# Kernel tuning notes

Hardware: AMD Instinct MI355X
Metric: run time of the kernel (lower is better)

The kernel has to match this reference:

```python
import jax, jax.numpy as jnp
import numpy as np

B, L, V, A = 4096, 64, 50000, 1000
E, H, G, F2 = 32, 32, 256, 512


def _xavier(k, shape):
    fan_out, fan_in = shape
    a = np.sqrt(6.0 / (fan_in + fan_out)).astype(np.float32)
    return jax.random.uniform(k, shape, jnp.float32, -a, a)


def setup_inputs() -> dict:
    key = jax.random.key(0)
    ks = jax.random.split(key, 32)
    inp = {}
    inp["q"] = jax.random.randint(ks[0], (B, L), 0, V)
    for i in range(8):
        inp[f"sf{i}"] = jax.random.randint(ks[1 + i], (B, L), 0, V)
    inp["emb"] = _xavier(ks[9], (V, E))
    # torch LSTM weight layout: [4H, in] with gate order i,f,g,o; biases init to 0
    inp["q_Wih"] = _xavier(ks[10], (4 * H, E))
    inp["q_Whh"] = _xavier(ks[11], (4 * H, H))
    inp["q_b"] = jnp.zeros((4 * H,), jnp.float32)
    inp["sf_Wih"] = _xavier(ks[12], (4 * H, E))
    inp["sf_Whh"] = _xavier(ks[13], (4 * H, H))
    inp["sf_b"] = jnp.zeros((4 * H,), jnp.float32)
    inp["g1_W"] = _xavier(ks[14], (G, 2 * H + 1)); inp["g1_b"] = jnp.zeros((G,), jnp.float32)
    inp["g2_W"] = _xavier(ks[15], (G, G)); inp["g2_b"] = jnp.zeros((G,), jnp.float32)
    inp["g3_W"] = _xavier(ks[16], (G, G)); inp["g3_b"] = jnp.zeros((G,), jnp.float32)
    inp["g4_W"] = _xavier(ks[17], (G, G)); inp["g4_b"] = jnp.zeros((G,), jnp.float32)
    inp["f1_W"] = _xavier(ks[18], (G, G)); inp["f1_b"] = jnp.zeros((G,), jnp.float32)
    inp["f2_W"] = _xavier(ks[19], (F2, G)); inp["f2_b"] = jnp.zeros((F2,), jnp.float32)
    inp["f3_W"] = _xavier(ks[20], (A, F2)); inp["f3_b"] = jnp.zeros((A,), jnp.float32)
    return inp


def _lstm_last(x, Wih, Whh, b):
    """x: [L, N, E] -> final hidden state [N, H]. Torch gate order i,f,g,o."""
    n = x.shape[1]
    h_dim = Whh.shape[1]
    def step(carry, xt):
        h, c = carry
        gates = xt @ Wih.T + h @ Whh.T + b  # [N, 4H]
        i, f, g, o = jnp.split(gates, 4, axis=-1)
        c = jax.nn.sigmoid(f) * c + jax.nn.sigmoid(i) * jnp.tanh(g)
        h = jax.nn.sigmoid(o) * jnp.tanh(c)
        return (h, c), None
    init = (jnp.zeros((n, h_dim), x.dtype), jnp.zeros((n, h_dim), x.dtype))
    (h, _), _ = jax.lax.scan(step, init, x)
    return h


def _lin(x, W, b):
    return x @ W.T + b


def reference(q, sf0, sf1, sf2, sf3, sf4, sf5, sf6, sf7,
              emb, q_Wih, q_Whh, q_b, sf_Wih, sf_Whh, sf_b,
              g1_W, g1_b, g2_W, g2_b, g3_W, g3_b, g4_W, g4_b,
              f1_W, f1_b, f2_W, f2_b, f3_W, f3_b):
    # dropout in eval mode (identity)
    b, l = q.shape
    qe = emb[q].transpose(1, 0, 2)  # [L, B, E]
    hq = _lstm_last(qe, q_Wih, q_Whh, q_b)  # [B, H]

    sf = jnp.stack([sf0, sf1, sf2, sf3, sf4, sf5, sf6, sf7])  # [8, B, L]
    sfe = emb[sf]  # [8, B, L, E]
    sfe = sfe.transpose(2, 0, 1, 3).reshape(l, 8 * b, emb.shape[1])  # one fused LSTM over 8*B
    hs = _lstm_last(sfe, sf_Wih, sf_Whh, sf_b).reshape(8, b, -1)  # [8, B, H]

    pos = jnp.broadcast_to(jnp.arange(8, dtype=hs.dtype)[:, None, None], (8, b, 1))
    x = jnp.concatenate([hs, jnp.broadcast_to(hq, (8, b, hq.shape[-1])), pos], axis=-1)  # [8, B, 65]
    x = jax.nn.relu(_lin(x, g1_W, g1_b))
    x = jax.nn.relu(_lin(x, g2_W, g2_b))
    x = jax.nn.relu(_lin(x, g3_W, g3_b))
    x = jax.nn.relu(_lin(x, g4_W, g4_b))
    g_o = x.sum(axis=0)  # [B, 256] segment-sum over the 8 relations

    x = jax.nn.relu(_lin(g_o, f1_W, f1_b))
    x = jax.nn.relu(_lin(x, f2_W, f2_b))
    return _lin(x, f3_W, f3_b)  # [B, A]
```

## Files before the change

kernel.cpp:

```cpp
#include <hip/hip_runtime.h>
#include <stdint.h>
#include <stddef.h>

typedef __fp16 f16;
typedef __attribute__((ext_vector_type(8))) __fp16 half8;
typedef __attribute__((ext_vector_type(4))) __fp16 half4;
typedef __attribute__((ext_vector_type(4))) float f32x4;

static __device__ __forceinline__ f32x4 mfma16(half8 a, half8 b, f32x4 c) {
    return __builtin_amdgcn_mfma_f32_16x16x32_f16(a, b, c, 0, 0, 0);
}
static __device__ __forceinline__ float fexp2(float x) { float r; asm("v_exp_f32 %0, %1" : "=v"(r) : "v"(x)); return r; }
static __device__ __forceinline__ float frcp(float x)  { float r; asm("v_rcp_f32 %0, %1" : "=v"(r) : "v"(x)); return r; }

static constexpr float L2E  = 1.4426950408889634f;
static constexpr float L2E2 = 2.8853900817779268f;

static constexpr int LD256 = 280;
static constexpr int LD512 = 536;

static constexpr size_t OFF_EMB   = 0;
static constexpr size_t OFF_WQIH  = 3200000;
static constexpr size_t OFF_WQHH  = OFF_WQIH + 8192;
static constexpr size_t OFF_WSIH  = OFF_WQHH + 8192;
static constexpr size_t OFF_WSHH  = OFF_WSIH + 8192;
static constexpr size_t OFF_BQ    = OFF_WSHH + 8192;
static constexpr size_t OFF_BS    = OFF_BQ + 512;
static constexpr size_t OFF_G1WP  = OFF_BS + 512;
static constexpr size_t OFF_BIAS8 = OFF_G1WP + 32768;
static constexpr size_t OFF_G2W   = OFF_BIAS8 + 8192;
static constexpr size_t OFF_G3W   = OFF_G2W + 131072;
static constexpr size_t OFF_G4W   = OFF_G3W + 131072;
static constexpr size_t OFF_F1W   = OFF_G4W + 131072;
static constexpr size_t OFF_F2W   = OFF_F1W + 131072;
static constexpr size_t OFF_F3W   = OFF_F2W + 262144;
static constexpr size_t OFF_HS    = OFF_F3W + 1024000;
static constexpr size_t OFF_HQ    = OFF_HS + 2097152;
static constexpr size_t OFF_ACT2  = OFF_HQ + 262144;
static constexpr size_t WS_NEED   = OFF_ACT2 + 16777216;

struct CvtJobs { const float* src[7]; f16* dst[7]; int n[7]; };

__global__ __launch_bounds__(256) void cvt_prep(
    CvtJobs j,
    const float* __restrict__ g1W, const float* __restrict__ g1b,
    f16* __restrict__ wp, float* __restrict__ bias8,
    const float* __restrict__ qWih, const float* __restrict__ qWhh, const float* __restrict__ qb,
    const float* __restrict__ sWih, const float* __restrict__ sWhh, const float* __restrict__ sb,
    f16* __restrict__ wqih, f16* __restrict__ wqhh, float* __restrict__ bq,
    f16* __restrict__ wsih, f16* __restrict__ wshh, float* __restrict__ bs)
{
    int t = threadIdx.x;
    if (blockIdx.y < 7) {
        int jb = blockIdx.y;
        int i = (blockIdx.x * 256 + t) * 8;
        if (i >= j.n[jb]) return;
        const float* s = j.src[jb] + i;
        f32x4 a = *(const f32x4*)s;
        f32x4 b = *(const f32x4*)(s + 4);
        half8 o;
        o[0]=(f16)a[0]; o[1]=(f16)a[1]; o[2]=(f16)a[2]; o[3]=(f16)a[3];
        o[4]=(f16)b[0]; o[5]=(f16)b[1]; o[6]=(f16)b[2]; o[7]=(f16)b[3];
        *(half8*)(j.dst[jb] + i) = o;
        return;
    }
    if (blockIdx.x == 0) {
        int col = t;
        for (int k = 0; k < 64; k++) wp[col * 64 + k] = (f16)g1W[col * 65 + k];
        float wpos = g1W[col * 65 + 64];
        float b = g1b[col];
        for (int i = 0; i < 8; i++) bias8[i * 256 + col] = b + (float)i * wpos;
    } else if (blockIdx.x == 1) {
        for (int i = t; i < 4096; i += 256) {
            int row = i >> 5;
            float s = (row < 64 || row >= 96) ? -L2E : L2E2;
            wqih[i] = (f16)(qWih[i] * s);
            wqhh[i] = (f16)(qWhh[i] * s);
            wsih[i] = (f16)(sWih[i] * s);
            wshh[i] = (f16)(sWhh[i] * s);
        }
        if (t < 128) {
            float s = (t < 64 || t >= 96) ? -L2E : L2E2;
            bq[t] = qb[t] * s;
            bs[t] = sb[t] * s;
        }
    }
}

struct SfPtrs { const int* p[8]; };

__global__ __launch_bounds__(64) void lstm_kernel(
    SfPtrs sf, const int* __restrict__ qtok, const f16* __restrict__ emb_h,
    const f16* __restrict__ wih_sf, const f16* __restrict__ whh_sf, const float* __restrict__ b_sf,
    const f16* __restrict__ wih_q,  const f16* __restrict__ whh_q,  const float* __restrict__ b_q,
    f16* __restrict__ hs_out, f16* __restrict__ hq_out)
{
    __shared__ __align__(16) char hb[16 * 80];
    int lane = threadIdx.x;
    int c15 = lane & 15, kq = lane >> 4;
    int sbase = blockIdx.x * 16;
    bool isq = sbase >= 32768;
    const f16* wih = isq ? wih_q : wih_sf;
    const f16* whh = isq ? whh_q : whh_sf;
    const float* bvec = isq ? b_q : b_sf;

    half8 wi[8], wh[8];
    f32x4 bc[8];
    #pragma unroll
    for (int n = 0; n < 8; n++) {
        wi[n] = *(const half8*)(wih + (n * 16 + c15) * 32 + kq * 8);
        wh[n] = *(const half8*)(whh + (n * 16 + c15) * 32 + kq * 8);
        bc[n] = *(const f32x4*)(bvec + n * 16 + kq * 4);
    }
    int sg = sbase + c15;
    const int* tp;
    if (isq) tp = qtok + (sg - 32768) * 64;
    else     tp = sf.p[sg >> 12] + (sg & 4095) * 64;

    f32x4 zro = {0.f, 0.f, 0.f, 0.f};
    *(f32x4*)(hb + lane * 16) = zro;
    if (lane < 16) *(f32x4*)(hb + 1024 + lane * 16) = zro;

    float cst[2][4] = {};
    const char* hrd = hb + c15 * 80 + kq * 16;

    int tok = tp[0];
    half8 xf = *(const half8*)(emb_h + (size_t)tok * 32 + kq * 8);

    #pragma unroll 1
    for (int t = 0; t < 64; t++) {
        half8 hf = *(const half8*)hrd;
        f32x4 acc[8];
        #pragma unroll
        for (int n = 0; n < 8; n++) acc[n] = mfma16(wi[n], xf, bc[n]);
        #pragma unroll
        for (int n = 0; n < 8; n++) acc[n] = mfma16(wh[n], hf, acc[n]);
        if (t < 63) {
            int tk = tp[t + 1];
            xf = *(const half8*)(emb_h + (size_t)tk * 32 + kq * 8);
        }
        #pragma unroll
        for (int jh = 0; jh < 2; jh++) {
            half4 hp;
            #pragma unroll
            for (int r = 0; r < 4; r++) {
                float ei = fexp2(acc[0 + jh][r]);
                float ef = fexp2(acc[2 + jh][r]);
                float eg = fexp2(acc[4 + jh][r]);
                float eo = fexp2(acc[6 + jh][r]);
                float t1 = 1.f + ei, t2 = 1.f + ef, t5 = 1.f + eo;
                float eg1 = eg + 1.f, egm = eg - 1.f;
                float num = fmaf(egm, t2, cst[jh][r] * t1 * eg1);
                float den = (t2 * t1) * eg1;
                float cn  = num * frcp(den);
                cst[jh][r] = cn;
                float ec  = fexp2(cn * L2E2);
                float hv  = (ec - 1.f) * frcp((ec + 1.f) * t5);
                hp[r] = (f16)hv;
            }
            *(half4*)(hb + c15 * 80 + jh * 32 + kq * 8) = hp;
        }
    }
    half8 hv = *(const half8*)hrd;
    if (isq) *(half8*)(hq_out + (size_t)(sg - 32768) * 32 + kq * 8) = hv;
    else     *(half8*)(hs_out + (size_t)sg * 32 + kq * 8) = hv;
}

template<bool TOGLOBAL>
static __device__ __forceinline__ void layer256(
    const f16 (* __restrict__ src)[LD256], f16 (* __restrict__ dst)[LD256],
    const f16* __restrict__ W, const float* __restrict__ bias,
    f16* __restrict__ gout, int m0, int wv, int c15, int kq)
{
    f32x4 acc[2][4];
    #pragma unroll
    for (int a = 0; a < 2; a++)
        #pragma unroll
        for (int b = 0; b < 4; b++) acc[a][b] = (f32x4){0.f, 0.f, 0.f, 0.f};
    #pragma unroll
    for (int k0 = 0; k0 < 8; k0++) {
        half8 av[2], bv[4];
        #pragma unroll
        for (int fm = 0; fm < 2; fm++) av[fm] = *(const half8*)(&src[fm * 16 + c15][k0 * 32 + kq * 8]);
        #pragma unroll
        for (int fn = 0; fn < 4; fn++) bv[fn] = *(const half8*)(W + (size_t)(wv * 64 + fn * 16 + c15) * 256 + k0 * 32 + kq * 8);
        #pragma unroll
        for (int fm = 0; fm < 2; fm++)
            #pragma unroll
            for (int fn = 0; fn < 4; fn++) acc[fm][fn] = mfma16(av[fm], bv[fn], acc[fm][fn]);
    }
    #pragma unroll
    for (int fn = 0; fn < 4; fn++) {
        int col = wv * 64 + fn * 16 + c15;
        float bb = bias[col];
        #pragma unroll
        for (int fm = 0; fm < 2; fm++)
            #pragma unroll
            for (int r = 0; r < 4; r++) {
                float v = fmaxf(acc[fm][fn][r] + bb, 0.f);
                if (TOGLOBAL) gout[(size_t)(m0 + fm * 16 + kq * 4 + r) * 256 + col] = (f16)v;
                else          dst[fm * 16 + kq * 4 + r][col] = (f16)v;
            }
    }
}

__global__ __launch_bounds__(256) void gemm_g1234(
    const f16* __restrict__ hs, const f16* __restrict__ hq,
    const f16* __restrict__ g1wp, const float* __restrict__ bias8,
    const f16* __restrict__ g2w, const float* __restrict__ g2b,
    const f16* __restrict__ g3w, const float* __restrict__ g3b,
    const f16* __restrict__ g4w, const float* __restrict__ g4b,
    f16* __restrict__ act2)
{
    __shared__ __align__(16) f16 actA[32][LD256];
    __shared__ __align__(16) f16 actB[32][LD256];
    const int wv = threadIdx.x >> 6, lane = threadIdx.x & 63;
    const int c15 = lane & 15, kq = lane >> 4;
    const int m0 = blockIdx.x * 32;
    const float* brow = bias8 + ((m0 >> 12) << 8);

    {
        f32x4 acc[2][4];
        #pragma unroll
        for (int a = 0; a < 2; a++)
            #pragma unroll
            for (int b = 0; b < 4; b++) acc[a][b] = (f32x4){0.f, 0.f, 0.f, 0.f};
        half8 av[2], bv[4];
        #pragma unroll
        for (int fm = 0; fm < 2; fm++) av[fm] = *(const half8*)(hs + (size_t)(m0 + fm * 16 + c15) * 32 + kq * 8);
        #pragma unroll
        for (int fn = 0; fn < 4; fn++) bv[fn] = *(const half8*)(g1wp + (size_t)(wv * 64 + fn * 16 + c15) * 64 + kq * 8);
        #pragma unroll
        for (int fm = 0; fm < 2; fm++)
            #pragma unroll
            for (int fn = 0; fn < 4; fn++) acc[fm][fn] = mfma16(av[fm], bv[fn], acc[fm][fn]);
        #pragma unroll
        for (int fm = 0; fm < 2; fm++) av[fm] = *(const half8*)(hq + (size_t)((m0 + fm * 16 + c15) & 4095) * 32 + kq * 8);
        #pragma unroll
        for (int fn = 0; fn < 4; fn++) bv[fn] = *(const half8*)(g1wp + (size_t)(wv * 64 + fn * 16 + c15) * 64 + 32 + kq * 8);
        #pragma unroll
        for (int fm = 0; fm < 2; fm++)
            #pragma unroll
            for (int fn = 0; fn < 4; fn++) acc[fm][fn] = mfma16(av[fm], bv[fn], acc[fm][fn]);
        #pragma unroll
        for (int fn = 0; fn < 4; fn++) {
            int col = wv * 64 + fn * 16 + c15;
            float bb = brow[col];
            #pragma unroll
            for (int fm = 0; fm < 2; fm++)
                #pragma unroll
                for (int r = 0; r < 4; r++)
                    actA[fm * 16 + kq * 4 + r][col] = (f16)fmaxf(acc[fm][fn][r] + bb, 0.f);
        }
    }
    __syncthreads();
    layer256<false>(actA, actB, g2w, g2b, nullptr, m0, wv, c15, kq);
    __syncthreads();
    layer256<false>(actB, actA, g3w, g3b, nullptr, m0, wv, c15, kq);
    __syncthreads();
    layer256<true>(actA, actB, g4w, g4b, act2, m0, wv, c15, kq);
}

__global__ __launch_bounds__(256) void f123s_kernel(
    const f16* __restrict__ act2,
    const f16* __restrict__ f1w, const float* __restrict__ f1b,
    const f16* __restrict__ f2w, const float* __restrict__ f2b,
    const f16* __restrict__ f3w, const float* __restrict__ f3b,
    float* __restrict__ out)
{
    __shared__ __align__(16) f16 smbuf[16][LD256];
    __shared__ __align__(16) f16 f1buf[16][LD256];
    __shared__ __align__(16) f16 f2buf[16][LD512];
    const int b0 = blockIdx.x * 16;

    {
        int r = threadIdx.x >> 4, cb = (threadIdx.x & 15) * 16;
        float s[16] = {};
        #pragma unroll
        for (int i = 0; i < 8; i++) {
            const f16* p = act2 + ((size_t)(i * 4096 + b0 + r)) * 256 + cb;
            half8 v0 = *(const half8*)p;
            half8 v1 = *(const half8*)(p + 8);
            #pragma unroll
            for (int q = 0; q < 8; q++) { s[q] += (float)v0[q]; s[8 + q] += (float)v1[q]; }
        }
        half8 o0, o1;
        #pragma unroll
        for (int q = 0; q < 8; q++) { o0[q] = (f16)s[q]; o1[q] = (f16)s[8 + q]; }
        *(half8*)(&smbuf[r][cb]) = o0;
        *(half8*)(&smbuf[r][cb + 8]) = o1;
    }
    __syncthreads();
    const int wv = threadIdx.x >> 6, lane = threadIdx.x & 63;
    const int c15 = lane & 15, kq = lane >> 4;

    {
        f32x4 acc[4];
        #pragma unroll
        for (int b = 0; b < 4; b++) acc[b] = (f32x4){0.f, 0.f, 0.f, 0.f};
        #pragma unroll
        for (int k0 = 0; k0 < 8; k0++) {
            half8 a = *(const half8*)(&smbuf[c15][k0 * 32 + kq * 8]);
            #pragma unroll
            for (int fn = 0; fn < 4; fn++) {
                half8 bv = *(const half8*)(f1w + (size_t)(wv * 64 + fn * 16 + c15) * 256 + k0 * 32 + kq * 8);
                acc[fn] = mfma16(a, bv, acc[fn]);
            }
        }
        #pragma unroll
        for (int fn = 0; fn < 4; fn++) {
            int col = wv * 64 + fn * 16 + c15;
            float bb = f1b[col];
            #pragma unroll
            for (int r = 0; r < 4; r++)
                f1buf[kq * 4 + r][col] = (f16)fmaxf(acc[fn][r] + bb, 0.f);
        }
    }
    __syncthreads();
    {
        f32x4 acc[8];
        #pragma unroll
        for (int b = 0; b < 8; b++) acc[b] = (f32x4){0.f, 0.f, 0.f, 0.f};
        #pragma unroll
        for (int k0 = 0; k0 < 8; k0++) {
            half8 a = *(const half8*)(&f1buf[c15][k0 * 32 + kq * 8]);
            #pragma unroll
            for (int fn = 0; fn < 8; fn++) {
                half8 bv = *(const half8*)(f2w + (size_t)(wv * 128 + fn * 16 + c15) * 256 + k0 * 32 + kq * 8);
                acc[fn] = mfma16(a, bv, acc[fn]);
            }
        }
        #pragma unroll
        for (int fn = 0; fn < 8; fn++) {
            int col = wv * 128 + fn * 16 + c15;
            float bb = f2b[col];
            #pragma unroll
            for (int r = 0; r < 4; r++)
                f2buf[kq * 4 + r][col] = (f16)fmaxf(acc[fn][r] + bb, 0.f);
        }
    }
    __syncthreads();
    {
        f32x4 acc[16];
        #pragma unroll
        for (int b = 0; b < 16; b++) acc[b] = (f32x4){0.f, 0.f, 0.f, 0.f};
        #pragma unroll
        for (int k0 = 0; k0 < 16; k0++) {
            half8 a = *(const half8*)(&f2buf[c15][k0 * 32 + kq * 8]);
            #pragma unroll
            for (int jj = 0; jj < 16; jj++) {
                int col = (wv + 4 * jj) * 16 + c15;
                int cl = col < 1000 ? col : 999;
                half8 bv = *(const half8*)(f3w + (size_t)cl * 512 + k0 * 32 + kq * 8);
                acc[jj] = mfma16(a, bv, acc[jj]);
            }
        }
        #pragma unroll
        for (int jj = 0; jj < 16; jj++) {
            int col = (wv + 4 * jj) * 16 + c15;
            if (col < 1000) {
                float bb = f3b[col];
                #pragma unroll
                for (int r = 0; r < 4; r++)
                    out[(size_t)(b0 + kq * 4 + r) * 1000 + col] = acc[jj][r] + bb;
            }
        }
    }
}

extern "C" void kernel_launch(void* const* d_in, const int* in_sizes, int n_in,
                              void* d_out, int out_size, void* d_ws, size_t ws_size,
                              hipStream_t stream)
{
    if (ws_size < WS_NEED) return;
    const int* q_tok = (const int*)d_in[0];
    SfPtrs sf;
    for (int i = 0; i < 8; i++) sf.p[i] = (const int*)d_in[1 + i];
    const float* emb_f = (const float*)d_in[9];
    const float* qWih = (const float*)d_in[10];
    const float* qWhh = (const float*)d_in[11];
    const float* q_b  = (const float*)d_in[12];
    const float* sWih = (const float*)d_in[13];
    const float* sWhh = (const float*)d_in[14];
    const float* s_b  = (const float*)d_in[15];
    const float* g1W  = (const float*)d_in[16];
    const float* g1b  = (const float*)d_in[17];
    const float* g2W  = (const float*)d_in[18];
    const float* g2b  = (const float*)d_in[19];
    const float* g3W  = (const float*)d_in[20];
    const float* g3b  = (const float*)d_in[21];
    const float* g4W  = (const float*)d_in[22];
    const float* g4b  = (const float*)d_in[23];
    const float* f1W  = (const float*)d_in[24];
    const float* f1b  = (const float*)d_in[25];
    const float* f2W  = (const float*)d_in[26];
    const float* f2b  = (const float*)d_in[27];
    const float* f3W  = (const float*)d_in[28];
    const float* f3b  = (const float*)d_in[29];

    char* ws = (char*)d_ws;
    f16* emb_h = (f16*)(ws + OFF_EMB);
    f16* wqih  = (f16*)(ws + OFF_WQIH);
    f16* wqhh  = (f16*)(ws + OFF_WQHH);
    f16* wsih  = (f16*)(ws + OFF_WSIH);
    f16* wshh  = (f16*)(ws + OFF_WSHH);
    float* bq  = (float*)(ws + OFF_BQ);
    float* bs  = (float*)(ws + OFF_BS);
    f16* g1wp  = (f16*)(ws + OFF_G1WP);
    float* bias8 = (float*)(ws + OFF_BIAS8);
    f16* g2w = (f16*)(ws + OFF_G2W);
    f16* g3w = (f16*)(ws + OFF_G3W);
    f16* g4w = (f16*)(ws + OFF_G4W);
    f16* f1w = (f16*)(ws + OFF_F1W);
    f16* f2w = (f16*)(ws + OFF_F2W);
    f16* f3w = (f16*)(ws + OFF_F3W);
    f16* hs  = (f16*)(ws + OFF_HS);
    f16* hq  = (f16*)(ws + OFF_HQ);
    f16* act2 = (f16*)(ws + OFF_ACT2);

    CvtJobs cj;
    const float* srcs[7] = {emb_f, g2W, g3W, g4W, f1W, f2W, f3W};
    f16* dsts[7]         = {emb_h, g2w, g3w, g4w, f1w, f2w, f3w};
    int ns[7] = {1600000, 65536, 65536, 65536, 65536, 131072, 512000};
    for (int i = 0; i < 7; i++) { cj.src[i] = srcs[i]; cj.dst[i] = dsts[i]; cj.n[i] = ns[i]; }

    cvt_prep<<<dim3(782, 8), 256, 0, stream>>>(cj, g1W, g1b, g1wp, bias8,
                                               qWih, qWhh, q_b, sWih, sWhh, s_b,
                                               wqih, wqhh, bq, wsih, wshh, bs);
    lstm_kernel<<<2304, 64, 0, stream>>>(sf, q_tok, emb_h, wsih, wshh, bs, wqih, wqhh, bq, hs, hq);
    gemm_g1234<<<1024, 256, 0, stream>>>(hs, hq, g1wp, bias8, g2w, g2b, g3w, g3b, g4w, g4b, act2);
    f123s_kernel<<<256, 256, 0, stream>>>(act2, f1w, f1b, f2w, f2b, f3w, f3b, (float*)d_out);
}
```

Measured before the change: 380.6 us.

## Interleave two LSTM sequence groups per wave and widen GEMM blocks to 512 threads

The LSTM kernel now processes two independent 16-sequence groups per wavefront, so two sets of MFMAs and gate math are interleaved to hide latency along the serial recurrence, and the grid is halved. The g1-g4 MLP kernel moves to 64-row tiles with 8 waves arranged 2x4, which reuses weight loads across more rows. The f123 kernel goes to 512 threads, splitting columns across 8 waves. LDS padding strides also change. The LSTM change doubles register pressure and halves the number of waves, which may reduce occupancy.

```diff
diff --git a/kernel.cpp b/kernel.cpp
--- a/kernel.cpp
+++ b/kernel.cpp
@@ -16,8 +16,8 @@
 static constexpr float L2E  = 1.4426950408889634f;
 static constexpr float L2E2 = 2.8853900817779268f;
 
-static constexpr int LD256 = 280;
-static constexpr int LD512 = 536;
+static constexpr int LDA = 264;
+static constexpr int LDF2 = 520;
 
 static constexpr size_t OFF_EMB   = 0;
 static constexpr size_t OFF_WQIH  = 3200000;
@@ -95,10 +95,11 @@
     const f16* __restrict__ wih_q,  const f16* __restrict__ whh_q,  const float* __restrict__ b_q,
     f16* __restrict__ hs_out, f16* __restrict__ hq_out)
 {
-    __shared__ __align__(16) char hb[16 * 80];
+    __shared__ __align__(16) char hb0[16 * 80];
+    __shared__ __align__(16) char hb1[16 * 80];
     int lane = threadIdx.x;
     int c15 = lane & 15, kq = lane >> 4;
-    int sbase = blockIdx.x * 16;
+    int sbase = blockIdx.x * 32;
     bool isq = sbase >= 32768;
     const f16* wih = isq ? wih_q : wih_sf;
     const f16* whh = isq ? whh_q : whh_sf;
@@ -112,65 +113,97 @@
         wh[n] = *(const half8*)(whh + (n * 16 + c15) * 32 + kq * 8);
         bc[n] = *(const f32x4*)(bvec + n * 16 + kq * 4);
     }
-    int sg = sbase + c15;
-    const int* tp;
-    if (isq) tp = qtok + (sg - 32768) * 64;
-    else     tp = sf.p[sg >> 12] + (sg & 4095) * 64;
+    int sg0 = sbase + c15, sg1 = sbase + 16 + c15;
+    const int* tp0; const int* tp1;
+    if (isq) { tp0 = qtok + (sg0 - 32768) * 64; tp1 = qtok + (sg1 - 32768) * 64; }
+    else     { tp0 = sf.p[sg0 >> 12] + (sg0 & 4095) * 64;
+               tp1 = sf.p[sg1 >> 12] + (sg1 & 4095) * 64; }
 
     f32x4 zro = {0.f, 0.f, 0.f, 0.f};
-    *(f32x4*)(hb + lane * 16) = zro;
-    if (lane < 16) *(f32x4*)(hb + 1024 + lane * 16) = zro;
-
-    float cst[2][4] = {};
-    const char* hrd = hb + c15 * 80 + kq * 16;
-
-    int tok = tp[0];
-    half8 xf = *(const half8*)(emb_h + (size_t)tok * 32 + kq * 8);
+    *(f32x4*)(hb0 + lane * 16) = zro;
+    *(f32x4*)(hb1 + lane * 16) = zro;
+    if (lane < 16) { *(f32x4*)(hb0 + 1024 + lane * 16) = zro;
+                     *(f32x4*)(hb1 + 1024 + lane * 16) = zro; }
+
+    float cst0[2][4] = {}, cst1[2][4] = {};
+    const char* hrd0 = hb0 + c15 * 80 + kq * 16;
+    const char* hrd1 = hb1 + c15 * 80 + kq * 16;
+
+    half8 xf0 = *(const half8*)(emb_h + (size_t)tp0[0] * 32 + kq * 8);
+    half8 xf1 = *(const half8*)(emb_h + (size_t)tp1[0] * 32 + kq * 8);
 
     #pragma unroll 1
     for (int t = 0; t < 64; t++) {
-        half8 hf = *(const half8*)hrd;
-        f32x4 acc[8];
-        #pragma unroll
-        for (int n = 0; n < 8; n++) acc[n] = mfma16(wi[n], xf, bc[n]);
-        #pragma unroll
-        for (int n = 0; n < 8; n++) acc[n] = mfma16(wh[n], hf, acc[n]);
+        half8 hf0 = *(const half8*)hrd0;
+        half8 hf1 = *(const half8*)hrd1;
+        f32x4 a0[8], a1[8];
+        #pragma unroll
+        for (int n = 0; n < 8; n++) a0[n] = mfma16(wi[n], xf0, bc[n]);
+        #pragma unroll
+        for (int n = 0; n < 8; n++) a1[n] = mfma16(wi[n], xf1, bc[n]);
+        #pragma unroll
+        for (int n = 0; n < 8; n++) a0[n] = mfma16(wh[n], hf0, a0[n]);
+        #pragma unroll
+        for (int n = 0; n < 8; n++) a1[n] = mfma16(wh[n], hf1, a1[n]);
         if (t < 63) {
-            int tk = tp[t + 1];
-            xf = *(const half8*)(emb_h + (size_t)tk * 32 + kq * 8);
+            xf0 = *(const half8*)(emb_h + (size_t)tp0[t + 1] * 32 + kq * 8);
+            xf1 = *(const half8*)(emb_h + (size_t)tp1[t + 1] * 32 + kq * 8);
         }
         #pragma unroll
         for (int jh = 0; jh < 2; jh++) {
             half4 hp;
             #pragma unroll
             for (int r = 0; r < 4; r++) {
-                float ei = fexp2(acc[0 + jh][r]);
-                float ef = fexp2(acc[2 + jh][r]);
-                float eg = fexp2(acc[4 + jh][r]);
-                float eo = fexp2(acc[6 + jh][r]);
+                float ei = fexp2(a0[0 + jh][r]);
+                float ef = fexp2(a0[2 + jh][r]);
+                float eg = fexp2(a0[4 + jh][r]);
+                float eo = fexp2(a0[6 + jh][r]);
                 float t1 = 1.f + ei, t2 = 1.f + ef, t5 = 1.f + eo;
                 float eg1 = eg + 1.f, egm = eg - 1.f;
-                float num = fmaf(egm, t2, cst[jh][r] * t1 * eg1);
-                float den = (t2 * t1) * eg1;
-                float cn  = num * frcp(den);
-                cst[jh][r] = cn;
+                float num = fmaf(egm, t2, cst0[jh][r] * t1 * eg1);
+                float cn  = num * frcp((t2 * t1) * eg1);
+                cst0[jh][r] = cn;
                 float ec  = fexp2(cn * L2E2);
-                float hv  = (ec - 1.f) * frcp((ec + 1.f) * t5);
-                hp[r] = (f16)hv;
-            }
-            *(half4*)(hb + c15 * 80 + jh * 32 + kq * 8) = hp;
-        }
-    }
-    half8 hv = *(const half8*)hrd;
-    if (isq) *(half8*)(hq_out + (size_t)(sg - 32768) * 32 + kq * 8) = hv;
-    else     *(half8*)(hs_out + (size_t)sg * 32 + kq * 8) = hv;
+                hp[r] = (f16)((ec - 1.f) * frcp((ec + 1.f) * t5));
+            }
+            *(half4*)(hb0 + c15 * 80 + jh * 32 + kq * 8) = hp;
+        }
+        #pragma unroll
+        for (int jh = 0; jh < 2; jh++) {
+            half4 hp;
+            #pragma unroll
+            for (int r = 0; r < 4; r++) {
+                float ei = fexp2(a1[0 + jh][r]);
+                float ef = fexp2(a1[2 + jh][r]);
+                float eg = fexp2(a1[4 + jh][r]);
+                float eo = fexp2(a1[6 + jh][r]);
+                float t1 = 1.f + ei, t2 = 1.f + ef, t5 = 1.f + eo;
+                float eg1 = eg + 1.f, egm = eg - 1.f;
+                float num = fmaf(egm, t2, cst1[jh][r] * t1 * eg1);
+                float cn  = num * frcp((t2 * t1) * eg1);
+                cst1[jh][r] = cn;
+                float ec  = fexp2(cn * L2E2);
+                hp[r] = (f16)((ec - 1.f) * frcp((ec + 1.f) * t5));
+            }
+            *(half4*)(hb1 + c15 * 80 + jh * 32 + kq * 8) = hp;
+        }
+    }
+    half8 hv0 = *(const half8*)hrd0;
+    half8 hv1 = *(const half8*)hrd1;
+    if (isq) {
+        *(half8*)(hq_out + (size_t)(sg0 - 32768) * 32 + kq * 8) = hv0;
+        *(half8*)(hq_out + (size_t)(sg1 - 32768) * 32 + kq * 8) = hv1;
+    } else {
+        *(half8*)(hs_out + (size_t)sg0 * 32 + kq * 8) = hv0;
+        *(half8*)(hs_out + (size_t)sg1 * 32 + kq * 8) = hv1;
+    }
 }
 
 template<bool TOGLOBAL>
 static __device__ __forceinline__ void layer256(
-    const f16 (* __restrict__ src)[LD256], f16 (* __restrict__ dst)[LD256],
+    const f16 (* __restrict__ src)[LDA], f16 (* __restrict__ dst)[LDA],
     const f16* __restrict__ W, const float* __restrict__ bias,
-    f16* __restrict__ gout, int m0, int wv, int c15, int kq)
+    f16* __restrict__ gout, int m0, int wm, int wn, int c15, int kq)
 {
     f32x4 acc[2][4];
     #pragma unroll
@@ -181,9 +214,9 @@
     for (int k0 = 0; k0 < 8; k0++) {
         half8 av[2], bv[4];
         #pragma unroll
-        for (int fm = 0; fm < 2; fm++) av[fm] = *(const half8*)(&src[fm * 16 + c15][k0 * 32 + kq * 8]);
-        #pragma unroll
-        for (int fn = 0; fn < 4; fn++) bv[fn] = *(const half8*)(W + (size_t)(wv * 64 + fn * 16 + c15) * 256 + k0 * 32 + kq * 8);
+        for (int fm = 0; fm < 2; fm++) av[fm] = *(const half8*)(&src[wm * 32 + fm * 16 + c15][k0 * 32 + kq * 8]);
+        #pragma unroll
+        for (int fn = 0; fn < 4; fn++) bv[fn] = *(const half8*)(W + (size_t)(wn * 64 + fn * 16 + c15) * 256 + k0 * 32 + kq * 8);
         #pragma unroll
         for (int fm = 0; fm < 2; fm++)
             #pragma unroll
@@ -191,20 +224,21 @@
     }
     #pragma unroll
     for (int fn = 0; fn < 4; fn++) {
-        int col = wv * 64 + fn * 16 + c15;
+        int col = wn * 64 + fn * 16 + c15;
         float bb = bias[col];
         #pragma unroll
         for (int fm = 0; fm < 2; fm++)
             #pragma unroll
             for (int r = 0; r < 4; r++) {
                 float v = fmaxf(acc[fm][fn][r] + bb, 0.f);
-                if (TOGLOBAL) gout[(size_t)(m0 + fm * 16 + kq * 4 + r) * 256 + col] = (f16)v;
-                else          dst[fm * 16 + kq * 4 + r][col] = (f16)v;
-            }
-    }
-}
-
-__global__ __launch_bounds__(256) void gemm_g1234(
+                int row = wm * 32 + fm * 16 + kq * 4 + r;
+                if (TOGLOBAL) gout[(size_t)(m0 + row) * 256 + col] = (f16)v;
+                else          dst[row][col] = (f16)v;
+            }
+    }
+}
+
+__global__ __launch_bounds__(512) void gemm_g1234(
     const f16* __restrict__ hs, const f16* __restrict__ hq,
     const f16* __restrict__ g1wp, const float* __restrict__ bias8,
     const f16* __restrict__ g2w, const float* __restrict__ g2b,
@@ -212,11 +246,12 @@
     const f16* __restrict__ g4w, const float* __restrict__ g4b,
     f16* __restrict__ act2)
 {
-    __shared__ __align__(16) f16 actA[32][LD256];
-    __shared__ __align__(16) f16 actB[32][LD256];
+    __shared__ __align__(16) f16 actA[64][LDA];
+    __shared__ __align__(16) f16 actB[64][LDA];
     const int wv = threadIdx.x >> 6, lane = threadIdx.x & 63;
     const int c15 = lane & 15, kq = lane >> 4;
-    const int m0 = blockIdx.x * 32;
+    const int wm = wv >> 2, wn = wv & 3;
+    const int m0 = blockIdx.x * 64;
     const float* brow = bias8 + ((m0 >> 12) << 8);
 
     {
@@ -227,93 +262,112 @@
             for (int b = 0; b < 4; b++) acc[a][b] = (f32x4){0.f, 0.f, 0.f, 0.f};
         half8 av[2], bv[4];
         #pragma unroll
-        for (int fm = 0; fm < 2; fm++) av[fm] = *(const half8*)(hs + (size_t)(m0 + fm * 16 + c15) * 32 + kq * 8);
-        #pragma unroll
-        for (int fn = 0; fn < 4; fn++) bv[fn] = *(const half8*)(g1wp + (size_t)(wv * 64 + fn * 16 + c15) * 64 + kq * 8);
+        for (int fm = 0; fm < 2; fm++) av[fm] = *(const half8*)(hs + (size_t)(m0 + wm * 32 + fm * 16 + c15) * 32 + kq * 8);
+        #pragma unroll
+        for (int fn = 0; fn < 4; fn++) bv[fn] = *(const half8*)(g1wp + (size_t)(wn * 64 + fn * 16 + c15) * 64 + kq * 8);
         #pragma unroll
         for (int fm = 0; fm < 2; fm++)
             #pragma unroll
             for (int fn = 0; fn < 4; fn++) acc[fm][fn] = mfma16(av[fm], bv[fn], acc[fm][fn]);
         #pragma unroll
-        for (int fm = 0; fm < 2; fm++) av[fm] = *(const half8*)(hq + (size_t)((m0 + fm * 16 + c15) & 4095) * 32 + kq * 8);
-        #pragma unroll
-        for (int fn = 0; fn < 4; fn++) bv[fn] = *(const half8*)(g1wp + (size_t)(wv * 64 + fn * 16 + c15) * 64 + 32 + kq * 8);
+        for (int fm = 0; fm < 2; fm++) av[fm] = *(const half8*)(hq + (size_t)((m0 + wm * 32 + fm * 16 + c15) & 4095) * 32 + kq * 8);
+        #pragma unroll
+        for (int fn = 0; fn < 4; fn++) bv[fn] = *(const half8*)(g1wp + (size_t)(wn * 64 + fn * 16 + c15) * 64 + 32 + kq * 8);
         #pragma unroll
         for (int fm = 0; fm < 2; fm++)
             #pragma unroll
             for (int fn = 0; fn < 4; fn++) acc[fm][fn] = mfma16(av[fm], bv[fn], acc[fm][fn]);
         #pragma unroll
         for (int fn = 0; fn < 4; fn++) {
-            int col = wv * 64 + fn * 16 + c15;
+            int col = wn * 64 + fn * 16 + c15;
             float bb = brow[col];
             #pragma unroll
             for (int fm = 0; fm < 2; fm++)
                 #pragma unroll
                 for (int r = 0; r < 4; r++)
-                    actA[fm * 16 + kq * 4 + r][col] = (f16)fmaxf(acc[fm][fn][r] + bb, 0.f);
-        }
-    }
-    __syncthreads();
-    layer256<false>(actA, actB, g2w, g2b, nullptr, m0, wv, c15, kq);
-    __syncthreads();
-    layer256<false>(actB, actA, g3w, g3b, nullptr, m0, wv, c15, kq);
-    __syncthreads();
-    layer256<true>(actA, actB, g4w, g4b, act2, m0, wv, c15, kq);
-}
-
-__global__ __launch_bounds__(256) void f123s_kernel(
+                    actA[wm * 32 + fm * 16 + kq * 4 + r][col] = (f16)fmaxf(acc[fm][fn][r] + bb, 0.f);
+        }
+    }
+    __syncthreads();
+    layer256<false>(actA, actB, g2w, g2b, nullptr, m0, wm, wn, c15, kq);
+    __syncthreads();
+    layer256<false>(actB, actA, g3w, g3b, nullptr, m0, wm, wn, c15, kq);
+    __syncthreads();
+    layer256<true>(actA, actB, g4w, g4b, act2, m0, wm, wn, c15, kq);
+}
+
+__global__ __launch_bounds__(512) void f123s_kernel(
     const f16* __restrict__ act2,
     const f16* __restrict__ f1w, const float* __restrict__ f1b,
     const f16* __restrict__ f2w, const float* __restrict__ f2b,
     const f16* __restrict__ f3w, const float* __restrict__ f3b,
     float* __restrict__ out)
 {
-    __shared__ __align__(16) f16 smbuf[16][LD256];
-    __shared__ __align__(16) f16 f1buf[16][LD256];
-    __shared__ __align__(16) f16 f2buf[16][LD512];
+    __shared__ __align__(16) f16 smbuf[16][LDA];
+    __shared__ __align__(16) f16 f1buf[16][LDA];
+    __shared__ __align__(16) f16 f2buf[16][LDF2];
     const int b0 = blockIdx.x * 16;
 
     {
-        int r = threadIdx.x >> 4, cb = (threadIdx.x & 15) * 16;
-        float s[16] = {};
+        int r = threadIdx.x >> 5, cb = (threadIdx.x & 31) * 8;
+        float s[8] = {};
         #pragma unroll
         for (int i = 0; i < 8; i++) {
-            const f16* p = act2 + ((size_t)(i * 4096 + b0 + r)) * 256 + cb;
-            half8 v0 = *(const half8*)p;
-            half8 v1 = *(const half8*)(p + 8);
-            #pragma unroll
-            for (int q = 0; q < 8; q++) { s[q] += (float)v0[q]; s[8 + q] += (float)v1[q]; }
-        }
-        half8 o0, o1;
-        #pragma unroll
-        for (int q = 0; q < 8; q++) { o0[q] = (f16)s[q]; o1[q] = (f16)s[8 + q]; }
-        *(half8*)(&smbuf[r][cb]) = o0;
-        *(half8*)(&smbuf[r][cb + 8]) = o1;
+            half8 v = *(const half8*)(act2 + ((size_t)(i * 4096 + b0 + r)) * 256 + cb);
+            #pragma unroll
+            for (int q = 0; q < 8; q++) s[q] += (float)v[q];
+        }
+        half8 o;
+        #pragma unroll
+        for (int q = 0; q < 8; q++) o[q] = (f16)s[q];
+        *(half8*)(&smbuf[r][cb]) = o;
     }
     __syncthreads();
     const int wv = threadIdx.x >> 6, lane = threadIdx.x & 63;
     const int c15 = lane & 15, kq = lane >> 4;
 
     {
-        f32x4 acc[4];
-        #pragma unroll
-        for (int b = 0; b < 4; b++) acc[b] = (f32x4){0.f, 0.f, 0.f, 0.f};
+        f32x4 acc[2];
+        acc[0] = (f32x4){0.f, 0.f, 0.f, 0.f}; acc[1] = acc[0];
         #pragma unroll
         for (int k0 = 0; k0 < 8; k0++) {
             half8 a = *(const half8*)(&smbuf[c15][k0 * 32 + kq * 8]);
             #pragma unroll
+            for (int fn = 0; fn < 2; fn++) {
+                half8 bv = *(const half8*)(f1w + (size_t)(wv * 32 + fn * 16 + c15) * 256 + k0 * 32 + kq * 8);
+                acc[fn] = mfma16(a, bv, acc[fn]);
+            }
+        }
+        #pragma unroll
+        for (int fn = 0; fn < 2; fn++) {
+            int col = wv * 32 + fn * 16 + c15;
+            float bb = f1b[col];
+            #pragma unroll
+            for (int r = 0; r < 4; r++)
+                f1buf[kq * 4 + r][col] = (f16)fmaxf(acc[fn][r] + bb, 0.f);
+        }
+    }
+    __syncthreads();
+    {
+        f32x4 acc[4];
+        #pragma unroll
+        for (int b = 0; b < 4; b++) acc[b] = (f32x4){0.f, 0.f, 0.f, 0.f};
+        #pragma unroll
+        for (int k0 = 0; k0 < 8; k0++) {
+            half8 a = *(const half8*)(&f1buf[c15][k0 * 32 + kq * 8]);
+            #pragma unroll
             for (int fn = 0; fn < 4; fn++) {
-                half8 bv = *(const half8*)(f1w + (size_t)(wv * 64 + fn * 16 + c15) * 256 + k0 * 32 + kq * 8);
+                half8 bv = *(const half8*)(f2w + (size_t)(wv * 64 + fn * 16 + c15) * 256 + k0 * 32 + kq * 8);
                 acc[fn] = mfma16(a, bv, acc[fn]);
             }
         }
         #pragma unroll
         for (int fn = 0; fn < 4; fn++) {
             int col = wv * 64 + fn * 16 + c15;
-            float bb = f1b[col];
+            float bb = f2b[col];
             #pragma unroll
             for (int r = 0; r < 4; r++)
-                f1buf[kq * 4 + r][col] = (f16)fmaxf(acc[fn][r] + bb, 0.f);
+                f2buf[kq * 4 + r][col] = (f16)fmaxf(acc[fn][r] + bb, 0.f);
         }
     }
     __syncthreads();
@@ -322,47 +376,24 @@
         #pragma unroll
         for (int b = 0; b < 8; b++) acc[b] = (f32x4){0.f, 0.f, 0.f, 0.f};
         #pragma unroll
-        for (int k0 = 0; k0 < 8; k0++) {
-            half8 a = *(const half8*)(&f1buf[c15][k0 * 32 + kq * 8]);
+        for (int k0 = 0; k0 < 16; k0++) {
+            half8 a = *(const half8*)(&f2buf[c15][k0 * 32 + kq * 8]);
             #pragma unroll
             for (int fn = 0; fn < 8; fn++) {
-                half8 bv = *(const half8*)(f2w + (size_t)(wv * 128 + fn * 16 + c15) * 256 + k0 * 32 + kq * 8);
+                int col = wv * 128 + fn * 16 + c15;
+                int cl = col < 1000 ? col : 999;
+                half8 bv = *(const half8*)(f3w + (size_t)cl * 512 + k0 * 32 + kq * 8);
                 acc[fn] = mfma16(a, bv, acc[fn]);
             }
         }
         #pragma unroll
         for (int fn = 0; fn < 8; fn++) {
             int col = wv * 128 + fn * 16 + c15;
-            float bb = f2b[col];
-            #pragma unroll
-            for (int r = 0; r < 4; r++)
-                f2buf[kq * 4 + r][col] = (f16)fmaxf(acc[fn][r] + bb, 0.f);
-        }
-    }
-    __syncthreads();
-    {
-        f32x4 acc[16];
-        #pragma unroll
-        for (int b = 0; b < 16; b++) acc[b] = (f32x4){0.f, 0.f, 0.f, 0.f};
-        #pragma unroll
-        for (int k0 = 0; k0 < 16; k0++) {
-            half8 a = *(const half8*)(&f2buf[c15][k0 * 32 + kq * 8]);
-            #pragma unroll
-            for (int jj = 0; jj < 16; jj++) {
-                int col = (wv + 4 * jj) * 16 + c15;
-                int cl = col < 1000 ? col : 999;
-                half8 bv = *(const half8*)(f3w + (size_t)cl * 512 + k0 * 32 + kq * 8);
-                acc[jj] = mfma16(a, bv, acc[jj]);
-            }
-        }
-        #pragma unroll
-        for (int jj = 0; jj < 16; jj++) {
-            int col = (wv + 4 * jj) * 16 + c15;
             if (col < 1000) {
                 float bb = f3b[col];
                 #pragma unroll
                 for (int r = 0; r < 4; r++)
-                    out[(size_t)(b0 + kq * 4 + r) * 1000 + col] = acc[jj][r] + bb;
+                    out[(size_t)(b0 + kq * 4 + r) * 1000 + col] = acc[fn][r] + bb;
             }
         }
     }
@@ -427,7 +458,7 @@
     cvt_prep<<<dim3(782, 8), 256, 0, stream>>>(cj, g1W, g1b, g1wp, bias8,
                                                qWih, qWhh, q_b, sWih, sWhh, s_b,
                                                wqih, wqhh, bq, wsih, wshh, bs);
-    lstm_kernel<<<2304, 64, 0, stream>>>(sf, q_tok, emb_h, wsih, wshh, bs, wqih, wqhh, bq, hs, hq);
-    gemm_g1234<<<1024, 256, 0, stream>>>(hs, hq, g1wp, bias8, g2w, g2b, g3w, g3b, g4w, g4b, act2);
-    f123s_kernel<<<256, 256, 0, stream>>>(act2, f1w, f1b, f2w, f2b, f3w, f3b, (float*)d_out);
-}
+    lstm_kernel<<<1152, 64, 0, stream>>>(sf, q_tok, emb_h, wsih, wshh, bs, wqih, wqhh, bq, hs, hq);
+    gemm_g1234<<<512, 512, 0, stream>>>(hs, hq, g1wp, bias8, g2w, g2b, g3w, g3b, g4w, g4b, act2);
+    f123s_kernel<<<256, 512, 0, stream>>>(act2, f1w, f1b, f2w, f2b, f3w, f3b, (float*)d_out);
+}
```

Result: slower. 394.1 us (+3.6%).
